# Kernel optimization log

Hardware: AMD Instinct MI355X
Metric: run time of the kernel (lower is better)

Reference implementation:

```python
import jax, jax.numpy as jnp
import numpy as np

# Config (matches init_kwargs)
B, S = 2, 2048            # 2 packed sequences of 2048 tokens (prefill)
HQ, HK, D = 32, 8, 128    # GQA: 32 query heads, 8 kv heads
G = HQ // HK              # group size 4
WINDOW = 1024             # sliding window
THETA = 10000.0


def setup_inputs() -> dict:
    key = jax.random.key(0)
    kq, kk, kv = jax.random.split(key, 3)
    n_tokens = B * S
    query = jax.random.normal(kq, (n_tokens, HQ * D), dtype=jnp.float32)
    key_t = jax.random.normal(kk, (n_tokens, HK * D), dtype=jnp.float32)
    value = jax.random.normal(kv, (n_tokens, HK * D), dtype=jnp.float32)
    # per-sequence positions restart at 0 for each packed sequence
    positions = jnp.tile(jnp.arange(S, dtype=jnp.int32), B)
    return {"query": query, "key": key_t, "value": value, "positions": positions}


def _rope(x, positions):
    # x: [B, S, H, D]; rotate-half (NeoX) RoPE
    half = D // 2
    inv_freq = 1.0 / (THETA ** (jnp.arange(0, half, dtype=jnp.float32) / half))
    ang = positions.astype(jnp.float32)[:, None] * inv_freq[None, :]   # [B*S, D/2]
    cos = jnp.cos(ang).reshape(B, S, 1, half)
    sin = jnp.sin(ang).reshape(B, S, 1, half)
    x1, x2 = x[..., :half], x[..., half:]
    return jnp.concatenate([x1 * cos - x2 * sin, x2 * cos + x1 * sin], axis=-1)


def reference(query, key, value, positions):
    q = query.reshape(B, S, HQ, D)
    k = key.reshape(B, S, HK, D)
    v = value.reshape(B, S, HK, D)
    q = _rope(q, positions)
    k = _rope(k, positions)
    # GQA: split q heads into [HK, G]
    qg = q.reshape(B, S, HK, G, D)
    scale = 1.0 / jnp.sqrt(jnp.float32(D))
    # scores: [B, HK, G, Sq, Skv]
    scores = jnp.einsum('bqhgd,bshd->bhgqs', qg, k) * scale
    i = jnp.arange(S)[:, None]
    j = jnp.arange(S)[None, :]
    # causal + sliding window: j <= i and i - j < WINDOW
    mask = (j <= i) & ((i - j) < WINDOW)
    scores = jnp.where(mask[None, None, None], scores, jnp.float32(-1e30))
    attn = jax.nn.softmax(scores, axis=-1)
    out = jnp.einsum('bhgqs,bshd->bqhgd', attn, v)   # [B, Sq, HK, G, D]
    return out.reshape(B * S, HQ * D)
```

## Files before the change

kernel.cpp:

```cpp
#include <hip/hip_runtime.h>
#include <stdint.h>

#define NB 2
#define NS 2048
#define NHK 8
#define ND 128
#define NWIN 1024

using bf16x8 = __bf16 __attribute__((ext_vector_type(8)));
using f32x4  = float  __attribute__((ext_vector_type(4)));
using f32x2  = float  __attribute__((ext_vector_type(2)));
using f32x8  = float  __attribute__((ext_vector_type(8)));
using u16x8  = unsigned short __attribute__((ext_vector_type(8)));
using u32x4  = unsigned int   __attribute__((ext_vector_type(4)));

#define L2_10K (13.287712379549449f / 64.0f)
#define MASKV (-3.0e38f)

static __device__ __forceinline__ float ex2(float x) {
  return __builtin_amdgcn_exp2f(x);
}

static __device__ __forceinline__ unsigned short f2bf(float x) {
  unsigned int u = __builtin_bit_cast(unsigned int, x);
  u += 0x7FFFu + ((u >> 16) & 1u);
  return (unsigned short)(u >> 16);
}

static __device__ __forceinline__ unsigned int cvtpk(float lo, float hi) {
  unsigned int r;
  asm("v_cvt_pk_bf16_f32 %0, %1, %2" : "=v"(r) : "v"(lo), "v"(hi));
  return r;
}

static __device__ __forceinline__ void gll16(const void* g, void* l) {
  __builtin_amdgcn_global_load_lds(
      (const __attribute__((address_space(1))) void*)g,
      (__attribute__((address_space(3))) void*)l, 16, 0, 0);
}

#define MFMA16(a, b, c) __builtin_amdgcn_mfma_f32_16x16x32_bf16((a), (b), (c), 0, 0, 0)

#define ROR(x, N) __builtin_bit_cast(float, __builtin_amdgcn_mov_dpp( \
    __builtin_bit_cast(int, (x)), 0x120 + (N), 0xF, 0xF, false))

__global__ __launch_bounds__(64) void build_tab(float* __restrict__ tab) {
  const int p = blockIdx.x, f = threadIdx.x;
  float s, c;
  __sincosf((float)p * ex2(-(float)f * L2_10K), &s, &c);
  tab[(size_t)p * 128 + f] = c;
  tab[(size_t)p * 128 + 64 + f] = s;
}

__global__ __launch_bounds__(256) void prepass(
    const float* __restrict__ kin, const float* __restrict__ vin,
    const int* __restrict__ pos, const float* __restrict__ tab,
    unsigned short* __restrict__ kimg, unsigned short* __restrict__ vimg) {
  const int bid = blockIdx.x;
  const int ti = bid & 63, gidx = bid >> 6;
  const int hk = gidx & 7, b = gidx >> 3;
  const int t = threadIdx.x;

  unsigned short* kout = kimg + (size_t)bid * 4096;
#pragma unroll
  for (int uu = 0; uu < 2; ++uu) {
    const int u = t * 2 + uu;
    const int j = u >> 4;
    const int d0 = ((u & 15) << 3) ^ ((j & 7) << 3);
    const int tok = (b << 11) + (ti << 5) + j;
    const float* kp = kin + (size_t)tok * (NHK * ND) + hk * ND;
    f32x8 a = *(const f32x8*)(kp + d0);
    f32x8 p = *(const f32x8*)(kp + (d0 ^ 64));
    const float* tr = tab + (size_t)(pos[tok] & 2047) * 128 + (d0 & 63);
    f32x8 c8 = *(const f32x8*)tr;
    f32x8 s8 = *(const f32x8*)(tr + 64);
    u16x8 o;
#pragma unroll
    for (int i = 0; i < 8; ++i) {
      float val = (d0 < 64) ? (a[i] * c8[i] - p[i] * s8[i])
                            : (a[i] * c8[i] + p[i] * s8[i]);
      o[i] = f2bf(val);
    }
    *(u16x8*)(kout + (size_t)u * 8) = o;
  }

  unsigned short* vout = vimg + (size_t)bid * 4096;
  {
    const int d0 = (t >> 2) << 1;
    const int kp4 = t & 3;
    const int tok0 = (b << 11) + (ti << 5) + (kp4 << 3);
    const float* vp = vin + (size_t)tok0 * (NHK * ND) + hk * ND + d0;
    u16x8 lo, hi;
#pragma unroll
    for (int i = 0; i < 8; ++i) {
      f32x2 r = *(const f32x2*)(vp + (size_t)i * (NHK * ND));
      lo[i] = f2bf(r[0]);
      hi[i] = f2bf(r[1]);
    }
    const int sub = kp4 ^ ((d0 >> 1) & 3);
    *(u16x8*)(vout + d0 * 32 + sub * 8) = lo;
    *(u16x8*)(vout + (d0 + 1) * 32 + sub * 8) = hi;
  }
}

template <bool PRE>
__global__ __launch_bounds__(256, 3) void attn_fwd(
    const float* __restrict__ qin, const float* __restrict__ kin,
    const float* __restrict__ vin, const int* __restrict__ pos,
    const char* __restrict__ kimg, const char* __restrict__ vimg,
    const float* __restrict__ tab, float* __restrict__ out) {
  __shared__ __align__(16) char Kb[2][8192];
  __shared__ __align__(16) char Vb[3][8192];

  const int B = blockIdx.x;
  const int group = (B & 7) + ((B >> 9) << 3);
  const int qt = 63 - ((B >> 3) & 63);
  const int hk = group & 7, b = group >> 3;

  const int tid = threadIdx.x;
  const int w = tid >> 6, lane = tid & 63, h = lane >> 4, ln = lane & 15;
  const int g = w;
  const int q0b = qt << 5;
  int lo = q0b - (NWIN - 1);
  if (lo < 0) lo = 0;
  lo &= ~31;
  const int ti0 = lo >> 5;
  const int nt = (q0b >> 5) - ti0 + 1;

  const size_t gbase = (size_t)group * 64 * 8192;
  const char* kg = PRE ? kimg + gbase + (size_t)(w * 128 + lane) * 16 : nullptr;
  const char* vg = PRE ? vimg + gbase + (size_t)(w * 128 + lane) * 16 : nullptr;

  auto stage = [&](int ks, int vs, int ti) {
    if constexpr (PRE) {
      const char* ksrc = kg + (size_t)ti * 8192;
      const char* vsrc = vg + (size_t)ti * 8192;
      char* kd = &Kb[ks][w * 2048];
      char* vd = &Vb[vs][w * 2048];
      gll16(ksrc, kd);
      gll16(ksrc + 1024, kd + 1024);
      gll16(vsrc, vd);
      gll16(vsrc + 1024, vd + 1024);
    } else {
      const int j = tid >> 3;
      const int du = (tid & 7) << 4;
      const int tok = (b << 11) + (ti << 5) + j;
      const float* kp = kin + (size_t)tok * (NHK * ND) + hk * ND;
      const float pj = (float)pos[tok];
#pragma unroll
      for (int gq = 0; gq < 2; ++gq) {
        const int dd = du + gq * 8;
        f32x8 a = *(const f32x8*)(kp + dd);
        f32x8 p = *(const f32x8*)(kp + (dd ^ 64));
        u16x8 o;
#pragma unroll
        for (int i = 0; i < 8; ++i) {
          float s, c;
          __sincosf(pj * ex2(-(float)((dd & 63) + i) * L2_10K), &s, &c);
          float val = (dd < 64) ? (a[i] * c - p[i] * s) : (a[i] * c + p[i] * s);
          o[i] = f2bf(val);
        }
        *(u16x8*)(&Kb[ks][((j << 8) + (dd << 1)) ^ ((j & 7) << 4)]) = o;
      }
      const int d0 = (tid >> 2) << 1;
      const int kp4 = tid & 3;
      const float* vp = vin + (size_t)((b << 11) + (ti << 5) + (kp4 << 3)) * (NHK * ND) + hk * ND + d0;
      u16x8 lov, hiv;
#pragma unroll
      for (int i = 0; i < 8; ++i) {
        f32x2 r = *(const f32x2*)(vp + (size_t)i * (NHK * ND));
        lov[i] = f2bf(r[0]);
        hiv[i] = f2bf(r[1]);
      }
      const int sub = kp4 ^ ((d0 >> 1) & 3);
      unsigned short* vb16 = (unsigned short*)Vb[vs];
      *(u16x8*)(vb16 + d0 * 32 + sub * 8) = lov;
      *(u16x8*)(vb16 + (d0 + 1) * 32 + sub * 8) = hiv;
    }
  };

  stage(0, 0, ti0);

  const float QSC = 0.08838834764831845f * 1.4426950408889634f;
  bf16x8 qfr[2][4];
#pragma unroll
  for (int hf = 0; hf < 2; ++hf) {
    const int qrow = q0b + hf * 16 + ln;
    const size_t tokq = (size_t)(b << 11) + qrow;
    const float* qp = qin + tokq * 4096 + (hk * 4 + g) * 128;
    const int posq = pos[tokq] & 2047;
#pragma unroll
    for (int pp = 0; pp < 2; ++pp) {
      const int rr = (pp << 5) + (h << 3);
      f32x8 lo8 = *(const f32x8*)(qp + rr);
      f32x8 hi8 = *(const f32x8*)(qp + rr + 64);
      f32x8 cc, ss;
      if constexpr (PRE) {
        const float* tp = tab + (size_t)posq * 128 + rr;
        cc = *(const f32x8*)tp;
        ss = *(const f32x8*)(tp + 64);
      } else {
        const float pf = (float)posq;
#pragma unroll
        for (int i = 0; i < 8; ++i) {
          float s, c;
          __sincosf(pf * ex2(-(float)(rr + i) * L2_10K), &s, &c);
          cc[i] = c;
          ss[i] = s;
        }
      }
      u16x8 ulo, uhi;
#pragma unroll
      for (int i = 0; i < 8; ++i) {
        ulo[i] = f2bf((lo8[i] * cc[i] - hi8[i] * ss[i]) * QSC);
        uhi[i] = f2bf((hi8[i] * cc[i] + lo8[i] * ss[i]) * QSC);
      }
      qfr[hf][pp] = __builtin_bit_cast(bf16x8, ulo);
      qfr[hf][2 + pp] = __builtin_bit_cast(bf16x8, uhi);
    }
  }

  f32x4 Oc[2][8] = {};
  float msh[2] = {-1e30f, -1e30f};
  float lsum[2] = {};
  bf16x8 pap0, pap1;
  const int sw = (ln & 7) << 4;
  const int vsub = (h ^ ((ln >> 1) & 3)) << 4;
  int vsp = 2, vsc = 0, vsn = 1;

  for (int t = 0; t < nt; ++t) {
    asm volatile("s_waitcnt vmcnt(0)" ::: "memory");
    __syncthreads();
    if (t + 1 < nt) stage((t + 1) & 1, vsn, ti0 + t + 1);

    const int j0 = (ti0 + t) << 5;
    const char* KB = Kb[t & 1];
    const char* VB = Vb[vsp];

    __builtin_amdgcn_s_setprio(1);
    if (t > 0) {
#pragma unroll
      for (int db = 0; db < 8; ++db) {
        const bf16x8 vv = *(const bf16x8*)(VB + (db << 10) + (ln << 6) + vsub);
        Oc[0][db] = MFMA16(pap0, vv, Oc[0][db]);
        Oc[1][db] = MFMA16(pap1, vv, Oc[1][db]);
      }
    }
    f32x4 sT[2][2] = {};
#pragma unroll
    for (int c = 0; c < 4; ++c) {
      const bf16x8 k0 = *(const bf16x8*)(
          KB + (((ln << 8) + (c << 6) + (h << 4)) ^ sw));
      const bf16x8 k1 = *(const bf16x8*)(
          KB + ((((16 + ln) << 8) + (c << 6) + (h << 4)) ^ sw));
      sT[0][0] = MFMA16(k0, qfr[0][c], sT[0][0]);
      sT[0][1] = MFMA16(k1, qfr[0][c], sT[0][1]);
      sT[1][0] = MFMA16(k0, qfr[1][c], sT[1][0]);
      sT[1][1] = MFMA16(k1, qfr[1][c], sT[1][1]);
    }
    __builtin_amdgcn_s_setprio(0);

    if ((j0 >= q0b) || (j0 < q0b - 992)) {
#pragma unroll
      for (int qh = 0; qh < 2; ++qh) {
        const int irow = q0b + qh * 16 + ln;
#pragma unroll
        for (int ki = 0; ki < 2; ++ki)
#pragma unroll
          for (int r = 0; r < 4; ++r) {
            const int j = j0 + ki * 16 + (h << 2) + r;
            if (!(j <= irow && irow - j < NWIN)) sT[qh][ki][r] = MASKV;
          }
      }
    }

    float pm[2];
#pragma unroll
    for (int qh = 0; qh < 2; ++qh) {
      const f32x4 s0 = sT[qh][0], s1 = sT[qh][1];
      pm[qh] = fmaxf(fmaxf(fmaxf(s0[0], s0[1]), fmaxf(s0[2], s0[3])),
                     fmaxf(fmaxf(s1[0], s1[1]), fmaxf(s1[2], s1[3])));
    }
    const float ov = fmaxf(pm[0] - msh[0], pm[1] - msh[1]);
    if (__any(ov > 8.0f)) {
#pragma unroll
      for (int qh = 0; qh < 2; ++qh) {
        float M = pm[qh];
        M = fmaxf(M, __shfl_xor(M, 16));
        M = fmaxf(M, __shfl_xor(M, 32));
        const float mn = fmaxf(msh[qh], M);
        const float co = ex2(msh[qh] - mn);
        msh[qh] = mn;
        lsum[qh] *= co;
        float coO[4];
#pragma unroll
        for (int r = 0; r < 4; ++r) coO[r] = __shfl(co, (h << 2) + r);
#pragma unroll
        for (int db = 0; db < 8; ++db)
#pragma unroll
          for (int r = 0; r < 4; ++r) Oc[qh][db][r] *= coO[r];
      }
    }
#pragma unroll
    for (int qh = 0; qh < 2; ++qh) {
#pragma unroll
      for (int ki = 0; ki < 2; ++ki)
#pragma unroll
        for (int r = 0; r < 4; ++r)
          sT[qh][ki][r] = ex2(sT[qh][ki][r] - msh[qh]);
      lsum[qh] += ((sT[qh][0][0] + sT[qh][0][1]) + (sT[qh][0][2] + sT[qh][0][3])) +
                  ((sT[qh][1][0] + sT[qh][1][1]) + (sT[qh][1][2] + sT[qh][1][3]));
      unsigned int A = cvtpk(sT[qh][0][0], sT[qh][0][1]);
      unsigned int Bk = cvtpk(sT[qh][0][2], sT[qh][0][3]);
      unsigned int C = cvtpk(sT[qh][1][0], sT[qh][1][1]);
      unsigned int D = cvtpk(sT[qh][1][2], sT[qh][1][3]);
      asm volatile("v_permlane32_swap_b32 %0, %1" : "+v"(A), "+v"(C));
      asm volatile("v_permlane16_swap_b32 %0, %1" : "+v"(A), "+v"(C));
      asm volatile("v_permlane32_swap_b32 %0, %1" : "+v"(Bk), "+v"(D));
      asm volatile("v_permlane16_swap_b32 %0, %1" : "+v"(Bk), "+v"(D));
      u32x4 pk4 = {A, Bk, C, D};
      if (qh == 0) pap0 = __builtin_bit_cast(bf16x8, pk4);
      else         pap1 = __builtin_bit_cast(bf16x8, pk4);
    }

    const int tmp = vsp;
    vsp = vsc; vsc = vsn; vsn = tmp;
  }

  {
    const char* VB = Vb[vsp];
#pragma unroll
    for (int db = 0; db < 8; ++db) {
      const bf16x8 vv = *(const bf16x8*)(VB + (db << 10) + (ln << 6) + vsub);
      Oc[0][db] = MFMA16(pap0, vv, Oc[0][db]);
      Oc[1][db] = MFMA16(pap1, vv, Oc[1][db]);
    }
  }

#pragma unroll
  for (int qh = 0; qh < 2; ++qh) {
    float ls = lsum[qh];
    ls += __shfl_xor(ls, 16);
    ls += __shfl_xor(ls, 32);
#pragma unroll
    for (int r = 0; r < 4; ++r) {
      const float rl = 1.0f / __shfl(ls, (h << 2) + r);
      const int irow = q0b + qh * 16 + (h << 2) + r;
      float* op = out + ((size_t)(b << 11) + irow) * 4096 + (hk * 4 + g) * 128 + ln;
#pragma unroll
      for (int db = 0; db < 8; ++db) op[db * 16] = Oc[qh][db][r] * rl;
    }
  }
}

extern "C" void kernel_launch(void* const* d_in, const int* in_sizes, int n_in,
                              void* d_out, int out_size, void* d_ws, size_t ws_size,
                              hipStream_t stream) {
  const float* q = (const float*)d_in[0];
  const float* k = (const float*)d_in[1];
  const float* v = (const float*)d_in[2];
  const int* pos = (const int*)d_in[3];
  float* out = (float*)d_out;

  const size_t TAB = (size_t)2048 * 128 * 4;
  const size_t KIMG = (size_t)16 * 64 * 8192;
  const size_t need = TAB + 2 * KIMG;

  if (ws_size >= need) {
    float* tab = (float*)d_ws;
    char* kimg = (char*)d_ws + TAB;
    char* vimg = kimg + KIMG;
    build_tab<<<2048, 64, 0, stream>>>(tab);
    prepass<<<1024, 256, 0, stream>>>(k, v, pos, tab,
                                      (unsigned short*)kimg, (unsigned short*)vimg);
    attn_fwd<true><<<1024, 256, 0, stream>>>(q, k, v, pos, kimg, vimg, tab, out);
  } else {
    attn_fwd<false><<<1024, 256, 0, stream>>>(q, k, v, pos, nullptr, nullptr, nullptr, out);
  }
}
```

Baseline: 95.23 us.

## Triple-buffer K/V tiles with two-ahead prefetch and in-iteration PV

K staging grows from double to triple buffering and K and V now share one rotating slot index. Loads run two tiles ahead, and the wait before each tile uses a partial vmcnt so the next tile's loads can stay in flight. The software-pipelined PV matmul, which consumed the previous tile's probabilities at the start of the next iteration, is removed; PV now runs in the same iteration right after softmax. This adds LDS (48KB per block, which may limit residency at 3 blocks per CU) and loses the overlap of PV with the next QK^T.

```diff
diff --git a/kernel.cpp b/kernel.cpp
--- a/kernel.cpp
+++ b/kernel.cpp
@@ -40,9 +40,6 @@
 }
 
 #define MFMA16(a, b, c) __builtin_amdgcn_mfma_f32_16x16x32_bf16((a), (b), (c), 0, 0, 0)
-
-#define ROR(x, N) __builtin_bit_cast(float, __builtin_amdgcn_mov_dpp( \
-    __builtin_bit_cast(int, (x)), 0x120 + (N), 0xF, 0xF, false))
 
 __global__ __launch_bounds__(64) void build_tab(float* __restrict__ tab) {
   const int p = blockIdx.x, f = threadIdx.x;
@@ -109,7 +106,7 @@
     const float* __restrict__ vin, const int* __restrict__ pos,
     const char* __restrict__ kimg, const char* __restrict__ vimg,
     const float* __restrict__ tab, float* __restrict__ out) {
-  __shared__ __align__(16) char Kb[2][8192];
+  __shared__ __align__(16) char Kb[3][8192];
   __shared__ __align__(16) char Vb[3][8192];
 
   const int B = blockIdx.x;
@@ -131,12 +128,12 @@
   const char* kg = PRE ? kimg + gbase + (size_t)(w * 128 + lane) * 16 : nullptr;
   const char* vg = PRE ? vimg + gbase + (size_t)(w * 128 + lane) * 16 : nullptr;
 
-  auto stage = [&](int ks, int vs, int ti) {
+  auto stage = [&](int sl, int ti) {
     if constexpr (PRE) {
       const char* ksrc = kg + (size_t)ti * 8192;
       const char* vsrc = vg + (size_t)ti * 8192;
-      char* kd = &Kb[ks][w * 2048];
-      char* vd = &Vb[vs][w * 2048];
+      char* kd = &Kb[sl][w * 2048];
+      char* vd = &Vb[sl][w * 2048];
       gll16(ksrc, kd);
       gll16(ksrc + 1024, kd + 1024);
       gll16(vsrc, vd);
@@ -160,7 +157,7 @@
           float val = (dd < 64) ? (a[i] * c - p[i] * s) : (a[i] * c + p[i] * s);
           o[i] = f2bf(val);
         }
-        *(u16x8*)(&Kb[ks][((j << 8) + (dd << 1)) ^ ((j & 7) << 4)]) = o;
+        *(u16x8*)(&Kb[sl][((j << 8) + (dd << 1)) ^ ((j & 7) << 4)]) = o;
       }
       const int d0 = (tid >> 2) << 1;
       const int kp4 = tid & 3;
@@ -173,13 +170,14 @@
         hiv[i] = f2bf(r[1]);
       }
       const int sub = kp4 ^ ((d0 >> 1) & 3);
-      unsigned short* vb16 = (unsigned short*)Vb[vs];
+      unsigned short* vb16 = (unsigned short*)Vb[sl];
       *(u16x8*)(vb16 + d0 * 32 + sub * 8) = lov;
       *(u16x8*)(vb16 + (d0 + 1) * 32 + sub * 8) = hiv;
     }
   };
 
-  stage(0, 0, ti0);
+  stage(0, ti0);
+  if (nt > 1) stage(1, ti0 + 1);
 
   const float QSC = 0.08838834764831845f * 1.4426950408889634f;
   bf16x8 qfr[2][4];
@@ -220,33 +218,31 @@
     }
   }
 
+  asm volatile("s_waitcnt vmcnt(0)" ::: "memory");
+
   f32x4 Oc[2][8] = {};
   float msh[2] = {-1e30f, -1e30f};
   float lsum[2] = {};
-  bf16x8 pap0, pap1;
   const int sw = (ln & 7) << 4;
   const int vsub = (h ^ ((ln >> 1) & 3)) << 4;
-  int vsp = 2, vsc = 0, vsn = 1;
+  int s0 = 0, s1 = 1, s2 = 2;
 
   for (int t = 0; t < nt; ++t) {
-    asm volatile("s_waitcnt vmcnt(0)" ::: "memory");
-    __syncthreads();
-    if (t + 1 < nt) stage((t + 1) & 1, vsn, ti0 + t + 1);
+    if constexpr (PRE) {
+      if (t + 1 < nt) asm volatile("s_waitcnt vmcnt(4)" ::: "memory");
+      else            asm volatile("s_waitcnt vmcnt(0)" ::: "memory");
+    } else {
+      asm volatile("s_waitcnt vmcnt(0) lgkmcnt(0)" ::: "memory");
+    }
+    __builtin_amdgcn_s_barrier();
+    __builtin_amdgcn_sched_barrier(0);
+    if (t + 2 < nt) stage(s2, ti0 + t + 2);
 
     const int j0 = (ti0 + t) << 5;
-    const char* KB = Kb[t & 1];
-    const char* VB = Vb[vsp];
-
+    const char* KB = Kb[s0];
+
+    f32x4 sT[2][2] = {};
     __builtin_amdgcn_s_setprio(1);
-    if (t > 0) {
-#pragma unroll
-      for (int db = 0; db < 8; ++db) {
-        const bf16x8 vv = *(const bf16x8*)(VB + (db << 10) + (ln << 6) + vsub);
-        Oc[0][db] = MFMA16(pap0, vv, Oc[0][db]);
-        Oc[1][db] = MFMA16(pap1, vv, Oc[1][db]);
-      }
-    }
-    f32x4 sT[2][2] = {};
 #pragma unroll
     for (int c = 0; c < 4; ++c) {
       const bf16x8 k0 = *(const bf16x8*)(
@@ -277,9 +273,9 @@
     float pm[2];
 #pragma unroll
     for (int qh = 0; qh < 2; ++qh) {
-      const f32x4 s0 = sT[qh][0], s1 = sT[qh][1];
-      pm[qh] = fmaxf(fmaxf(fmaxf(s0[0], s0[1]), fmaxf(s0[2], s0[3])),
-                     fmaxf(fmaxf(s1[0], s1[1]), fmaxf(s1[2], s1[3])));
+      const f32x4 a0 = sT[qh][0], a1 = sT[qh][1];
+      pm[qh] = fmaxf(fmaxf(fmaxf(a0[0], a0[1]), fmaxf(a0[2], a0[3])),
+                     fmaxf(fmaxf(a1[0], a1[1]), fmaxf(a1[2], a1[3])));
     }
     const float ov = fmaxf(pm[0] - msh[0], pm[1] - msh[1]);
     if (__any(ov > 8.0f)) {
@@ -301,6 +297,8 @@
           for (int r = 0; r < 4; ++r) Oc[qh][db][r] *= coO[r];
       }
     }
+
+    bf16x8 pa[2];
 #pragma unroll
     for (int qh = 0; qh < 2; ++qh) {
 #pragma unroll
@@ -319,22 +317,21 @@
       asm volatile("v_permlane32_swap_b32 %0, %1" : "+v"(Bk), "+v"(D));
       asm volatile("v_permlane16_swap_b32 %0, %1" : "+v"(Bk), "+v"(D));
       u32x4 pk4 = {A, Bk, C, D};
-      if (qh == 0) pap0 = __builtin_bit_cast(bf16x8, pk4);
-      else         pap1 = __builtin_bit_cast(bf16x8, pk4);
-    }
-
-    const int tmp = vsp;
-    vsp = vsc; vsc = vsn; vsn = tmp;
-  }
-
-  {
-    const char* VB = Vb[vsp];
+      pa[qh] = __builtin_bit_cast(bf16x8, pk4);
+    }
+
+    const char* VB = Vb[s0];
+    __builtin_amdgcn_s_setprio(1);
 #pragma unroll
     for (int db = 0; db < 8; ++db) {
       const bf16x8 vv = *(const bf16x8*)(VB + (db << 10) + (ln << 6) + vsub);
-      Oc[0][db] = MFMA16(pap0, vv, Oc[0][db]);
-      Oc[1][db] = MFMA16(pap1, vv, Oc[1][db]);
-    }
+      Oc[0][db] = MFMA16(pa[0], vv, Oc[0][db]);
+      Oc[1][db] = MFMA16(pa[1], vv, Oc[1][db]);
+    }
+    __builtin_amdgcn_s_setprio(0);
+
+    const int tmp = s0;
+    s0 = s1; s1 = s2; s2 = tmp;
   }
 
 #pragma unroll
```

New measurement: 95.92 us. About the same (+0.7%).
